# Kernel tuning notes

Measured on AMD Instinct MI355X. Metric: run time of the kernel, lower is better.

## Reference

```python
import jax, jax.numpy as jnp
import numpy as np

B, S, D = 4, 1024, 1024
H, DK, DV = 16, 64, 32
SCALE = float(np.sqrt(DK))


def setup_inputs() -> dict:
    key = jax.random.key(0)
    ks = jax.random.split(key, 10)
    std = 0.02
    x = jax.random.normal(ks[0], (B, S, D), dtype=jnp.float32)
    # Per-head projection weights stacked: y = x @ W + b (equiv to torch Linear)
    Wq = jax.random.normal(ks[1], (H, D, DK), dtype=jnp.float32) * std
    bq = jax.random.normal(ks[2], (H, DK), dtype=jnp.float32) * std
    Wk = jax.random.normal(ks[3], (H, D, DK), dtype=jnp.float32) * std
    bk = jax.random.normal(ks[4], (H, DK), dtype=jnp.float32) * std
    Wv = jax.random.normal(ks[5], (H, D, DV), dtype=jnp.float32) * std
    bv = jax.random.normal(ks[6], (H, DV), dtype=jnp.float32) * std
    Wo = jax.random.normal(ks[7], (H * DV, D), dtype=jnp.float32) * std
    bo = jax.random.normal(ks[8], (D,), dtype=jnp.float32) * std
    return {"x": x, "Wq": Wq, "bq": bq, "Wk": Wk, "bk": bk,
            "Wv": Wv, "bv": bv, "Wo": Wo, "bo": bo}


def reference(x, Wq, bq, Wk, bk, Wv, bv, Wo, bo):
    # batched per-head projections (vectorizes the torch per-head loop)
    q = jnp.einsum('bsd,hdk->bhsk', x, Wq) + bq[None, :, None, :]
    k = jnp.einsum('bsd,hdk->bhsk', x, Wk) + bk[None, :, None, :]
    v = jnp.einsum('bsd,hdv->bhsv', x, Wv) + bv[None, :, None, :]
    # scaled dot-product attention (no mask path)
    scores = jnp.einsum('bhsk,bhtk->bhst', q, k) / SCALE  # [B,H,S,S]
    weights = jax.nn.softmax(scores, axis=-1)
    out_h = jnp.einsum('bhst,bhtv->bhsv', weights, v)      # [B,H,S,DV]
    # concat heads in head order (matches torch.cat over head_outputs)
    concat = out_h.transpose(0, 2, 1, 3).reshape(B, S, H * DV)
    output = concat @ Wo + bo  # dropout p=0 / eval -> identity
    return (output, weights)
```

## Files before the change

### kernel.cpp

```cpp
#include <hip/hip_runtime.h>
#include <cstdint>
#include <cstddef>

#define BB 4
#define SS 1024
#define DD 1024
#define HH 16
#define DKK 64
#define DVV 32
#define LOG2E 1.44269504088896340736f

typedef __bf16 bf16_t;
typedef __bf16 bf16x8 __attribute__((ext_vector_type(8)));
typedef float f32x4 __attribute__((ext_vector_type(4)));

typedef __attribute__((address_space(3))) unsigned int lds_u32;
typedef const __attribute__((address_space(1))) unsigned int glb_u32;

__device__ inline bf16x8 cvt8(const float* __restrict__ s) {
  float4 a = *(const float4*)s;
  float4 b = *(const float4*)(s + 4);
  bf16x8 r;
  r[0] = (__bf16)a.x; r[1] = (__bf16)a.y; r[2] = (__bf16)a.z; r[3] = (__bf16)a.w;
  r[4] = (__bf16)b.x; r[5] = (__bf16)b.y; r[6] = (__bf16)b.z; r[7] = (__bf16)b.w;
  return r;
}

__global__ __launch_bounds__(256) void xcvt_kernel(
    const float* __restrict__ X, bf16_t* __restrict__ Xb) {
  size_t i = ((size_t)blockIdx.x * 256 + threadIdx.x) * 16;
  bf16x8 a = cvt8(X + i);
  bf16x8 b = cvt8(X + i + 8);
  *(bf16x8*)(Xb + i) = a;
  *(bf16x8*)(Xb + i + 8) = b;
}

__global__ __launch_bounds__(256) void transpose_cvt_kernel(
    const float* __restrict__ src, bf16_t* __restrict__ dst,
    int M, int N, size_t srcStride, size_t dstStride) {
  __shared__ __align__(16) bf16_t T[64][72];
  const int tid = threadIdx.x;
  const int n0 = blockIdx.x * 64, m0 = blockIdx.y * 64;
  const float* s = src + (size_t)blockIdx.z * srcStride;
  bf16_t* d = dst + (size_t)blockIdx.z * dstStride;
  const int rr = tid >> 3, c8 = (tid & 7) * 8;

  if (n0 + c8 < N) {
#pragma unroll
    for (int mm = rr; mm < 64; mm += 32) {
      const float* p = s + (size_t)(m0 + mm) * N + n0 + c8;
      float4 a = *(const float4*)p;
      float4 b = *(const float4*)(p + 4);
      T[c8 + 0][mm] = (__bf16)a.x; T[c8 + 1][mm] = (__bf16)a.y;
      T[c8 + 2][mm] = (__bf16)a.z; T[c8 + 3][mm] = (__bf16)a.w;
      T[c8 + 4][mm] = (__bf16)b.x; T[c8 + 5][mm] = (__bf16)b.y;
      T[c8 + 6][mm] = (__bf16)b.z; T[c8 + 7][mm] = (__bf16)b.w;
    }
  }
  __syncthreads();
#pragma unroll
  for (int rn = rr; rn < 64; rn += 32) {
    if (n0 + rn < N)
      *(uint4*)(d + (size_t)(n0 + rn) * M + m0 + c8) = *(uint4*)&T[rn][c8];
  }
}

__global__ __launch_bounds__(256) void wqkv_transpose_kernel(
    const float* __restrict__ Wq, const float* __restrict__ Wk,
    const float* __restrict__ Wv, bf16_t* __restrict__ WcatT) {
  __shared__ __align__(16) bf16_t T[64][72];
  const int tid = threadIdx.x;
  const int z = blockIdx.y;
  const float* s; bf16_t* d; int N;
  if (z < 16)      { s = Wq + (size_t)z * 65536;        d = WcatT + (size_t)z * 65536;                          N = 64; }
  else if (z < 32) { s = Wk + (size_t)(z - 16) * 65536; d = WcatT + (size_t)1024 * 1024 + (size_t)(z - 16) * 65536; N = 64; }
  else             { s = Wv + (size_t)(z - 32) * 32768; d = WcatT + (size_t)2048 * 1024 + (size_t)(z - 32) * 32768; N = 32; }
  const int m0 = blockIdx.x * 64;
  const int rr = tid >> 3, c8 = (tid & 7) * 8;

  if (c8 < N) {
#pragma unroll
    for (int mm = rr; mm < 64; mm += 32) {
      const float* p = s + (size_t)(m0 + mm) * N + c8;
      float4 a = *(const float4*)p;
      float4 b = *(const float4*)(p + 4);
      T[c8 + 0][mm] = (__bf16)a.x; T[c8 + 1][mm] = (__bf16)a.y;
      T[c8 + 2][mm] = (__bf16)a.z; T[c8 + 3][mm] = (__bf16)a.w;
      T[c8 + 4][mm] = (__bf16)b.x; T[c8 + 5][mm] = (__bf16)b.y;
      T[c8 + 6][mm] = (__bf16)b.z; T[c8 + 7][mm] = (__bf16)b.w;
    }
  }
  __syncthreads();
#pragma unroll
  for (int rn = rr; rn < 64; rn += 32) {
    if (rn < N)
      *(uint4*)(d + (size_t)rn * 1024 + m0 + c8) = *(uint4*)&T[rn][c8];
  }
}

__global__ __launch_bounds__(256) void qkv_gemm_kernel(
    const bf16_t* __restrict__ Xb, const bf16_t* __restrict__ WT,
    const float* __restrict__ bq, const float* __restrict__ bk,
    const float* __restrict__ bv,
    bf16_t* __restrict__ Qw, bf16_t* __restrict__ Kw, bf16_t* __restrict__ VT) {
  __shared__ __align__(16) bf16_t As[128 * 64];
  __shared__ __align__(16) bf16_t Bs[128 * 64];
  const int tid = threadIdx.x;
  const int wave = tid >> 6;
  const int lane = tid & 63;
  const int wr = wave >> 1, wc = wave & 1;
  const int g = lane >> 4, ln = lane & 15;
  const int m0 = blockIdx.x * 128;
  const int n0 = blockIdx.y * 128;
  const int srow = lane >> 3;
  const int scol = (lane & 7) * 8;

  f32x4 acc[4][4] = {};

  for (int k0 = 0; k0 < 1024; k0 += 64) {
#pragma unroll
    for (int c = 0; c < 4; c++) {
      const int rb = (wave * 4 + c) * 8;
      __builtin_amdgcn_global_load_lds(
          (glb_u32*)(Xb + (size_t)(m0 + rb + srow) * 1024 + k0 + scol),
          (lds_u32*)(As + rb * 64), 16, 0, 0);
      __builtin_amdgcn_global_load_lds(
          (glb_u32*)(WT + (size_t)(n0 + rb + srow) * 1024 + k0 + scol),
          (lds_u32*)(Bs + rb * 64), 16, 0, 0);
    }
    __syncthreads();
#pragma unroll
    for (int ks = 0; ks < 2; ks++) {
      bf16x8 a[4], b[4];
#pragma unroll
      for (int m = 0; m < 4; m++)
        a[m] = *(const bf16x8*)(As + (wr * 64 + m * 16 + ln) * 64 + ks * 32 + g * 8);
#pragma unroll
      for (int n = 0; n < 4; n++)
        b[n] = *(const bf16x8*)(Bs + (wc * 64 + n * 16 + ln) * 64 + ks * 32 + g * 8);
#pragma unroll
      for (int m = 0; m < 4; m++)
#pragma unroll
        for (int n = 0; n < 4; n++)
          acc[m][n] = __builtin_amdgcn_mfma_f32_16x16x32_bf16(a[m], b[n], acc[m][n], 0, 0, 0);
    }
    __syncthreads();
  }

  const int orow = m0 + wr * 64;
  const int ocol = n0 + wc * 64;
#pragma unroll
  for (int n = 0; n < 4; n++) {
    int c = ocol + n * 16 + ln;
    float bias = (c < 1024) ? bq[c] : (c < 2048 ? bk[c - 1024] : bv[c - 2048]);
#pragma unroll
    for (int m = 0; m < 4; m++) {
#pragma unroll
      for (int i = 0; i < 4; i++) {
        int mm = orow + m * 16 + g * 4 + i;
        float v = acc[m][n][i] + bias;
        int b_ = mm >> 10, s_ = mm & 1023;
        if (c < 1024) {
          int h = c >> 6, k = c & 63;
          Qw[(((size_t)(b_ * HH + h)) * SS + s_) * DKK + k] = (__bf16)(v * 0.125f);
        } else if (c < 2048) {
          int c2 = c - 1024, h = c2 >> 6, k = c2 & 63;
          Kw[(((size_t)(b_ * HH + h)) * SS + s_) * DKK + k] = (__bf16)v;
        } else {
          int c2 = c - 2048, h = c2 >> 5, vv = c2 & 31;
          VT[(((size_t)(b_ * HH + h)) * DVV + vv) * SS + s_] = (__bf16)v;
        }
      }
    }
  }
}

__global__ __launch_bounds__(256) void attn_fused_kernel(
    const bf16_t* __restrict__ Qw, const bf16_t* __restrict__ Kw,
    const bf16_t* __restrict__ VT, float* __restrict__ Wout,
    bf16_t* __restrict__ concat) {
  __shared__ __align__(16) bf16_t Qs[64][72];
  __shared__ __align__(16) bf16_t Ks[64][72];
  __shared__ __align__(16) bf16_t Ps[64][72];
  __shared__ __align__(16) bf16_t Vs[32][72];
  const int bh = blockIdx.y;
  const int b_ = bh >> 4, h = bh & 15;
  const int m0 = blockIdx.x * 64;
  const int tid = threadIdx.x;
  const int wave = tid >> 6;
  const int lane = tid & 63;
  const int g = lane >> 4;
  const int ln = lane & 15;
  const int r = tid >> 3;
  const int c8 = (tid & 7) * 8;

  const bf16_t* Qbase = Qw + (size_t)bh * SS * DKK;
  const bf16_t* Kbase = Kw + (size_t)bh * SS * DKK;
  const bf16_t* vbase = VT + (size_t)bh * DVV * SS;

  *(uint4*)&Qs[r][c8]      = *(const uint4*)(Qbase + (size_t)(m0 + r) * DKK + c8);
  *(uint4*)&Qs[r + 32][c8] = *(const uint4*)(Qbase + (size_t)(m0 + r + 32) * DKK + c8);

  float lrun[4] = {0.f, 0.f, 0.f, 0.f};

  uint4 ka = *(const uint4*)(Kbase + (size_t)r * DKK + c8);
  uint4 kb = *(const uint4*)(Kbase + (size_t)(r + 32) * DKK + c8);
  for (int jt = 0; jt < 16; jt++) {
    __syncthreads();
    *(uint4*)&Ks[r][c8]      = ka;
    *(uint4*)&Ks[r + 32][c8] = kb;
    if (jt + 1 < 16) {
      ka = *(const uint4*)(Kbase + (size_t)((jt + 1) * 64 + r) * DKK + c8);
      kb = *(const uint4*)(Kbase + (size_t)((jt + 1) * 64 + r + 32) * DKK + c8);
    }
    __syncthreads();
    f32x4 acc[4] = {};
#pragma unroll
    for (int ks = 0; ks < 2; ks++) {
      bf16x8 a = *(const bf16x8*)&Qs[wave * 16 + ln][ks * 32 + g * 8];
#pragma unroll
      for (int ns = 0; ns < 4; ns++) {
        bf16x8 b = *(const bf16x8*)&Ks[ns * 16 + ln][ks * 32 + g * 8];
        acc[ns] = __builtin_amdgcn_mfma_f32_16x16x32_bf16(a, b, acc[ns], 0, 0, 0);
      }
    }
#pragma unroll
    for (int ns = 0; ns < 4; ns++)
#pragma unroll
      for (int i = 0; i < 4; i++)
        lrun[i] += exp2f(acc[ns][i] * LOG2E);
  }

#pragma unroll
  for (int i = 0; i < 4; i++) {
    float l = lrun[i];
#pragma unroll
    for (int d = 1; d < 16; d <<= 1) l += __shfl_xor(l, d);
    lrun[i] = 1.0f / l;
  }

  float* wbase = Wout + (size_t)bh * SS * SS;
  f32x4 acc_o[2] = {};
  ka = *(const uint4*)(Kbase + (size_t)r * DKK + c8);
  kb = *(const uint4*)(Kbase + (size_t)(r + 32) * DKK + c8);
  uint4 va = *(const uint4*)(vbase + (size_t)r * SS + c8);
  for (int jt = 0; jt < 16; jt++) {
    __syncthreads();
    *(uint4*)&Ks[r][c8]      = ka;
    *(uint4*)&Ks[r + 32][c8] = kb;
    *(uint4*)&Vs[r][c8]      = va;
    if (jt + 1 < 16) {
      ka = *(const uint4*)(Kbase + (size_t)((jt + 1) * 64 + r) * DKK + c8);
      kb = *(const uint4*)(Kbase + (size_t)((jt + 1) * 64 + r + 32) * DKK + c8);
      va = *(const uint4*)(vbase + (size_t)r * SS + (jt + 1) * 64 + c8);
    }
    __syncthreads();
    f32x4 acc[4] = {};
#pragma unroll
    for (int ks = 0; ks < 2; ks++) {
      bf16x8 a = *(const bf16x8*)&Qs[wave * 16 + ln][ks * 32 + g * 8];
#pragma unroll
      for (int ns = 0; ns < 4; ns++) {
        bf16x8 b = *(const bf16x8*)&Ks[ns * 16 + ln][ks * 32 + g * 8];
        acc[ns] = __builtin_amdgcn_mfma_f32_16x16x32_bf16(a, b, acc[ns], 0, 0, 0);
      }
    }
#pragma unroll
    for (int ns = 0; ns < 4; ns++) {
      int col = jt * 64 + ns * 16 + ln;
#pragma unroll
      for (int i = 0; i < 4; i++) {
        int mr = wave * 16 + g * 4 + i;
        float w = exp2f(acc[ns][i] * LOG2E) * lrun[i];
        wbase[(size_t)(m0 + mr) * SS + col] = w;
        Ps[mr][ns * 16 + ln] = (__bf16)w;
      }
    }
#pragma unroll
    for (int ks = 0; ks < 2; ks++) {
      bf16x8 a = *(const bf16x8*)&Ps[wave * 16 + ln][ks * 32 + g * 8];
#pragma unroll
      for (int n2 = 0; n2 < 2; n2++) {
        bf16x8 b = *(const bf16x8*)&Vs[n2 * 16 + ln][ks * 32 + g * 8];
        acc_o[n2] = __builtin_amdgcn_mfma_f32_16x16x32_bf16(a, b, acc_o[n2], 0, 0, 0);
      }
    }
  }

#pragma unroll
  for (int n2 = 0; n2 < 2; n2++) {
    int col = n2 * 16 + ln;
#pragma unroll
    for (int i = 0; i < 4; i++) {
      int s_ = m0 + wave * 16 + g * 4 + i;
      concat[((size_t)(b_ * SS + s_)) * (HH * DVV) + h * DVV + col] =
          (__bf16)acc_o[n2][i];
    }
  }
}

__global__ __launch_bounds__(256) void out_gemm_kernel(
    const bf16_t* __restrict__ Cc, const bf16_t* __restrict__ WoT,
    const float* __restrict__ bo, float* __restrict__ Out) {
  __shared__ __align__(16) bf16_t As[128 * 64];
  __shared__ __align__(16) bf16_t Bs[128 * 64];
  const int tid = threadIdx.x;
  const int wave = tid >> 6;
  const int lane = tid & 63;
  const int wr = wave >> 1, wc = wave & 1;
  const int g = lane >> 4, ln = lane & 15;
  const int m0 = blockIdx.x * 128;
  const int n0 = blockIdx.y * 128;
  const int srow = lane >> 3;
  const int scol = (lane & 7) * 8;

  f32x4 acc[4][4] = {};

  for (int k0 = 0; k0 < 512; k0 += 64) {
#pragma unroll
    for (int c = 0; c < 4; c++) {
      const int rb = (wave * 4 + c) * 8;
      __builtin_amdgcn_global_load_lds(
          (glb_u32*)(Cc + (size_t)(m0 + rb + srow) * 512 + k0 + scol),
          (lds_u32*)(As + rb * 64), 16, 0, 0);
      __builtin_amdgcn_global_load_lds(
          (glb_u32*)(WoT + (size_t)(n0 + rb + srow) * 512 + k0 + scol),
          (lds_u32*)(Bs + rb * 64), 16, 0, 0);
    }
    __syncthreads();
#pragma unroll
    for (int ks = 0; ks < 2; ks++) {
      bf16x8 a[4], b[4];
#pragma unroll
      for (int m = 0; m < 4; m++)
        a[m] = *(const bf16x8*)(As + (wr * 64 + m * 16 + ln) * 64 + ks * 32 + g * 8);
#pragma unroll
      for (int n = 0; n < 4; n++)
        b[n] = *(const bf16x8*)(Bs + (wc * 64 + n * 16 + ln) * 64 + ks * 32 + g * 8);
#pragma unroll
      for (int m = 0; m < 4; m++)
#pragma unroll
        for (int n = 0; n < 4; n++)
          acc[m][n] = __builtin_amdgcn_mfma_f32_16x16x32_bf16(a[m], b[n], acc[m][n], 0, 0, 0);
    }
    __syncthreads();
  }

#pragma unroll
  for (int n = 0; n < 4; n++) {
    int col = n0 + wc * 64 + n * 16 + ln;
    float bias = bo[col];
#pragma unroll
    for (int m = 0; m < 4; m++) {
#pragma unroll
      for (int i = 0; i < 4; i++) {
        int mm = m0 + wr * 64 + m * 16 + g * 4 + i;
        Out[(size_t)mm * DD + col] = acc[m][n][i] + bias;
      }
    }
  }
}

extern "C" void kernel_launch(void* const* d_in, const int* in_sizes, int n_in,
                              void* d_out, int out_size, void* d_ws, size_t ws_size,
                              hipStream_t stream) {
  const float* x  = (const float*)d_in[0];
  const float* Wq = (const float*)d_in[1];
  const float* bq = (const float*)d_in[2];
  const float* Wk = (const float*)d_in[3];
  const float* bk = (const float*)d_in[4];
  const float* Wv = (const float*)d_in[5];
  const float* bv = (const float*)d_in[6];
  const float* Wo = (const float*)d_in[7];
  const float* bo = (const float*)d_in[8];

  float* out = (float*)d_out;
  float* weights_out = out + (size_t)BB * SS * DD;

  char* ws = (char*)d_ws;
  bf16_t* WcatT = (bf16_t*)ws;  ws += (size_t)2560 * 1024 * 2;
  bf16_t* WoT   = (bf16_t*)ws;  ws += (size_t)1024 * 512 * 2;
  bf16_t* Qw    = (bf16_t*)ws;  ws += (size_t)BB * HH * SS * DKK * 2;
  bf16_t* Kw    = (bf16_t*)ws;  ws += (size_t)BB * HH * SS * DKK * 2;
  bf16_t* VT    = (bf16_t*)ws;  ws += (size_t)BB * HH * DVV * SS * 2;
  bf16_t* concat = (bf16_t*)ws;

  bf16_t* Xb = (bf16_t*)weights_out;

  wqkv_transpose_kernel<<<dim3(16, 48), 256, 0, stream>>>(Wq, Wk, Wv, WcatT);
  transpose_cvt_kernel<<<dim3(16, 8, 1), 256, 0, stream>>>(
      Wo, WoT, 512, 1024, 0, 0);
  xcvt_kernel<<<1024, 256, 0, stream>>>(x, Xb);

  qkv_gemm_kernel<<<dim3(32, 20), 256, 0, stream>>>(
      Xb, WcatT, bq, bk, bv, Qw, Kw, VT);
  attn_fused_kernel<<<dim3(16, 64), 256, 0, stream>>>(
      Qw, Kw, VT, weights_out, concat);
  out_gemm_kernel<<<dim3(32, 8), 256, 0, stream>>>(concat, WoT, bo, out);
}
```

Before: 439.1 us.

## Swizzle block order for XCDs, add MFMA priority, nontemporal weight stores, smaller out-GEMM tiles

Flattens the grids of all three main kernels and remaps block ids so consecutive ids map round-robin across the 8 XCDs, grouping neighbouring tiles on the same XCD's L2. It brackets MFMA sections in the attention kernel with s_setprio to favour matrix issue. The attention-weights output is written with nontemporal stores so it does not pollute the cache. The output GEMM tile shrinks from 128x128 to 128x64, doubling the block count to improve occupancy and CU coverage at the cost of less reuse per block.

```diff
diff --git a/kernel.cpp b/kernel.cpp
--- a/kernel.cpp
+++ b/kernel.cpp
@@ -105,13 +105,15 @@
     bf16_t* __restrict__ Qw, bf16_t* __restrict__ Kw, bf16_t* __restrict__ VT) {
   __shared__ __align__(16) bf16_t As[128 * 64];
   __shared__ __align__(16) bf16_t Bs[128 * 64];
+  const int id = blockIdx.x;
+  const int swz = (id & 7) * 80 + (id >> 3);
+  const int m0 = (swz % 32) * 128;
+  const int n0 = (swz / 32) * 128;
   const int tid = threadIdx.x;
   const int wave = tid >> 6;
   const int lane = tid & 63;
   const int wr = wave >> 1, wc = wave & 1;
   const int g = lane >> 4, ln = lane & 15;
-  const int m0 = blockIdx.x * 128;
-  const int n0 = blockIdx.y * 128;
   const int srow = lane >> 3;
   const int scol = (lane & 7) * 8;
 
@@ -183,9 +185,11 @@
   __shared__ __align__(16) bf16_t Ks[64][72];
   __shared__ __align__(16) bf16_t Ps[64][72];
   __shared__ __align__(16) bf16_t Vs[32][72];
-  const int bh = blockIdx.y;
+  const int id = blockIdx.x;
+  const int swz = (id & 7) * 128 + (id >> 3);
+  const int bh = swz >> 4;
+  const int m0 = (swz & 15) * 64;
   const int b_ = bh >> 4, h = bh & 15;
-  const int m0 = blockIdx.x * 64;
   const int tid = threadIdx.x;
   const int wave = tid >> 6;
   const int lane = tid & 63;
@@ -215,6 +219,7 @@
     }
     __syncthreads();
     f32x4 acc[4] = {};
+    __builtin_amdgcn_s_setprio(1);
 #pragma unroll
     for (int ks = 0; ks < 2; ks++) {
       bf16x8 a = *(const bf16x8*)&Qs[wave * 16 + ln][ks * 32 + g * 8];
@@ -224,6 +229,7 @@
         acc[ns] = __builtin_amdgcn_mfma_f32_16x16x32_bf16(a, b, acc[ns], 0, 0, 0);
       }
     }
+    __builtin_amdgcn_s_setprio(0);
 #pragma unroll
     for (int ns = 0; ns < 4; ns++)
 #pragma unroll
@@ -256,6 +262,7 @@
     }
     __syncthreads();
     f32x4 acc[4] = {};
+    __builtin_amdgcn_s_setprio(1);
 #pragma unroll
     for (int ks = 0; ks < 2; ks++) {
       bf16x8 a = *(const bf16x8*)&Qs[wave * 16 + ln][ks * 32 + g * 8];
@@ -265,6 +272,7 @@
         acc[ns] = __builtin_amdgcn_mfma_f32_16x16x32_bf16(a, b, acc[ns], 0, 0, 0);
       }
     }
+    __builtin_amdgcn_s_setprio(0);
 #pragma unroll
     for (int ns = 0; ns < 4; ns++) {
       int col = jt * 64 + ns * 16 + ln;
@@ -272,10 +280,11 @@
       for (int i = 0; i < 4; i++) {
         int mr = wave * 16 + g * 4 + i;
         float w = exp2f(acc[ns][i] * LOG2E) * lrun[i];
-        wbase[(size_t)(m0 + mr) * SS + col] = w;
+        __builtin_nontemporal_store(w, wbase + (size_t)(m0 + mr) * SS + col);
         Ps[mr][ns * 16 + ln] = (__bf16)w;
       }
     }
+    __builtin_amdgcn_s_setprio(1);
 #pragma unroll
     for (int ks = 0; ks < 2; ks++) {
       bf16x8 a = *(const bf16x8*)&Ps[wave * 16 + ln][ks * 32 + g * 8];
@@ -285,6 +294,7 @@
         acc_o[n2] = __builtin_amdgcn_mfma_f32_16x16x32_bf16(a, b, acc_o[n2], 0, 0, 0);
       }
     }
+    __builtin_amdgcn_s_setprio(0);
   }
 
 #pragma unroll
@@ -303,18 +313,20 @@
     const bf16_t* __restrict__ Cc, const bf16_t* __restrict__ WoT,
     const float* __restrict__ bo, float* __restrict__ Out) {
   __shared__ __align__(16) bf16_t As[128 * 64];
-  __shared__ __align__(16) bf16_t Bs[128 * 64];
+  __shared__ __align__(16) bf16_t Bs[64 * 64];
+  const int id = blockIdx.x;
+  const int swz = (id & 7) * 64 + (id >> 3);
+  const int m0 = (swz & 31) * 128;
+  const int n0 = (swz >> 5) * 64;
   const int tid = threadIdx.x;
   const int wave = tid >> 6;
   const int lane = tid & 63;
   const int wr = wave >> 1, wc = wave & 1;
   const int g = lane >> 4, ln = lane & 15;
-  const int m0 = blockIdx.x * 128;
-  const int n0 = blockIdx.y * 128;
   const int srow = lane >> 3;
   const int scol = (lane & 7) * 8;
 
-  f32x4 acc[4][4] = {};
+  f32x4 acc[4][2] = {};
 
   for (int k0 = 0; k0 < 512; k0 += 64) {
 #pragma unroll
@@ -323,6 +335,10 @@
       __builtin_amdgcn_global_load_lds(
           (glb_u32*)(Cc + (size_t)(m0 + rb + srow) * 512 + k0 + scol),
           (lds_u32*)(As + rb * 64), 16, 0, 0);
+    }
+#pragma unroll
+    for (int c = 0; c < 2; c++) {
+      const int rb = (wave * 2 + c) * 8;
       __builtin_amdgcn_global_load_lds(
           (glb_u32*)(WoT + (size_t)(n0 + rb + srow) * 512 + k0 + scol),
           (lds_u32*)(Bs + rb * 64), 16, 0, 0);
@@ -330,25 +346,25 @@
     __syncthreads();
 #pragma unroll
     for (int ks = 0; ks < 2; ks++) {
-      bf16x8 a[4], b[4];
+      bf16x8 a[4], b[2];
 #pragma unroll
       for (int m = 0; m < 4; m++)
         a[m] = *(const bf16x8*)(As + (wr * 64 + m * 16 + ln) * 64 + ks * 32 + g * 8);
 #pragma unroll
-      for (int n = 0; n < 4; n++)
-        b[n] = *(const bf16x8*)(Bs + (wc * 64 + n * 16 + ln) * 64 + ks * 32 + g * 8);
+      for (int n = 0; n < 2; n++)
+        b[n] = *(const bf16x8*)(Bs + (wc * 32 + n * 16 + ln) * 64 + ks * 32 + g * 8);
 #pragma unroll
       for (int m = 0; m < 4; m++)
 #pragma unroll
-        for (int n = 0; n < 4; n++)
+        for (int n = 0; n < 2; n++)
           acc[m][n] = __builtin_amdgcn_mfma_f32_16x16x32_bf16(a[m], b[n], acc[m][n], 0, 0, 0);
     }
     __syncthreads();
   }
 
 #pragma unroll
-  for (int n = 0; n < 4; n++) {
-    int col = n0 + wc * 64 + n * 16 + ln;
+  for (int n = 0; n < 2; n++) {
+    int col = n0 + wc * 32 + n * 16 + ln;
     float bias = bo[col];
 #pragma unroll
     for (int m = 0; m < 4; m++) {
@@ -392,9 +408,9 @@
       Wo, WoT, 512, 1024, 0, 0);
   xcvt_kernel<<<1024, 256, 0, stream>>>(x, Xb);
 
-  qkv_gemm_kernel<<<dim3(32, 20), 256, 0, stream>>>(
+  qkv_gemm_kernel<<<640, 256, 0, stream>>>(
       Xb, WcatT, bq, bk, bv, Qw, Kw, VT);
-  attn_fused_kernel<<<dim3(16, 64), 256, 0, stream>>>(
+  attn_fused_kernel<<<1024, 256, 0, stream>>>(
       Qw, Kw, VT, weights_out, concat);
-  out_gemm_kernel<<<dim3(32, 8), 256, 0, stream>>>(concat, WoT, bo, out);
-}
+  out_gemm_kernel<<<512, 256, 0, stream>>>(concat, WoT, bo, out);
+}
```

Result: slower. 457.8 us (+4.3%).
